# Kernel optimization log

Hardware: AMD Instinct MI355X
Metric: run time of the kernel (lower is better)

Reference implementation:

```python
import jax, jax.numpy as jnp
import numpy as np

B, T, D, NH = 4, 2048, 768, 12
DH = D // NH
NEG = -100000.0  # module uses masked_fill with -100000.0, not -inf


def setup_inputs() -> dict:
    key = jax.random.key(0)
    ks = jax.random.split(key, 9)
    s = 1.0 / np.sqrt(D)
    return {
        "x": jax.random.normal(ks[0], (B, T, D), jnp.float32),
        "wq": jax.random.normal(ks[1], (D, D), jnp.float32) * s,
        "bq": jax.random.normal(ks[2], (D,), jnp.float32) * 0.02,
        "wk": jax.random.normal(ks[3], (D, D), jnp.float32) * s,
        "bk": jax.random.normal(ks[4], (D,), jnp.float32) * 0.02,
        "wv": jax.random.normal(ks[5], (D, D), jnp.float32) * s,
        "bv": jax.random.normal(ks[6], (D,), jnp.float32) * 0.02,
        "wo": jax.random.normal(ks[7], (D, D), jnp.float32) * s,
        "bo": jax.random.normal(ks[8], (D,), jnp.float32) * 0.02,
    }


def reference(x, wq, bq, wk, bk, wv, bv, wo, bo):
    Bx, Tx, E = x.shape
    # torch Linear: y = x @ W.T + b, weight shape [out, in]
    def heads(w, b):
        return (x @ w.T + b).reshape(Bx, Tx, NH, DH).transpose(0, 2, 1, 3)  # [B,nh,T,dh]
    Q, K, V = heads(wq, bq), heads(wk, bk), heads(wv, bv)
    scale = 1.0 / jnp.sqrt(jnp.float32(DH))
    QK = jnp.einsum("bhqd,bhkd->bhqk", Q, K) * scale  # [B,nh,T,T]
    causal = jnp.tril(jnp.ones((Tx, Tx), dtype=bool))
    QK = jnp.where(causal, QK, NEG)
    A = jax.nn.softmax(QK, axis=-1)  # attn_dropout p=0 (eval)
    Z = jnp.einsum("bhqk,bhkd->bhqd", A, V)
    Z = Z.transpose(0, 2, 1, 3).reshape(Bx, Tx, E)
    return Z @ wo.T + bo  # resid_dropout p=0 (eval)
```

## Files before the change

kernel.cpp:

```cpp
#include <hip/hip_runtime.h>


#define B_ 4
#define T_ 2048
#define D_ 768
#define NH_ 12
#define DH_ 64
#define M_ (B_ * T_)

typedef __attribute__((ext_vector_type(8))) short bf16x8;
typedef __attribute__((ext_vector_type(4))) float f32x4;
typedef __attribute__((ext_vector_type(16))) float f32x16;
typedef __attribute__((ext_vector_type(4))) unsigned int u32x4;

__device__ __forceinline__ unsigned short f2bf(float f) {
  unsigned int u = __builtin_bit_cast(unsigned int, f);
  u += 0x7FFFu + ((u >> 16) & 1u);
  return (unsigned short)(u >> 16);
}

__device__ __forceinline__ void async16(const void* g, void* l) {
  __builtin_amdgcn_global_load_lds(
      (const __attribute__((address_space(1))) unsigned int*)g,
      (__attribute__((address_space(3))) unsigned int*)l, 16, 0, 0);
}

#define RAW_BARRIER()                         \
  do {                                        \
    asm volatile("" ::: "memory");            \
    __builtin_amdgcn_s_barrier();             \
    asm volatile("" ::: "memory");            \
  } while (0)

__global__ void cvt_kernel(const float* __restrict__ x, const float* __restrict__ wq,
                           const float* __restrict__ wk, const float* __restrict__ wv,
                           const float* __restrict__ wo,
                           unsigned short* __restrict__ xb, unsigned short* __restrict__ wqb,
                           unsigned short* __restrict__ wkb, unsigned short* __restrict__ wvb,
                           unsigned short* __restrict__ wob) {
  const float* src; unsigned short* dst; int n4;
  switch (blockIdx.y) {
    case 0: src = x;  dst = xb;  n4 = M_ * D_ / 4; break;
    case 1: src = wq; dst = wqb; n4 = D_ * D_ / 4; break;
    case 2: src = wk; dst = wkb; n4 = D_ * D_ / 4; break;
    case 3: src = wv; dst = wvb; n4 = D_ * D_ / 4; break;
    default: src = wo; dst = wob; n4 = D_ * D_ / 4; break;
  }
  int stride = gridDim.x * blockDim.x;
  for (int i = blockIdx.x * blockDim.x + threadIdx.x; i < n4; i += stride) {
    float4 v = ((const float4*)src)[i];
    ushort4 o;
    o.x = f2bf(v.x); o.y = f2bf(v.y); o.z = f2bf(v.z); o.w = f2bf(v.w);
    ((ushort4*)dst)[i] = o;
  }
}

__global__ __launch_bounds__(512, 4) void gemm_kernel(
    const unsigned short* __restrict__ A,
    const unsigned short* __restrict__ W0, const unsigned short* __restrict__ W1,
    const unsigned short* __restrict__ W2,
    const float* __restrict__ bias0, const float* __restrict__ bias1,
    const float* __restrict__ bias2,
    void* out0, void* out1, void* out2,
    float s0, int K, int qkv) {
  __shared__ __align__(16) char lds[49152];

  int bid = blockIdx.x;
  int xcd = bid & 7, g = bid >> 3;
  int mt, nt;
  if (qkv) { mt = xcd + (g / 9) * 8; nt = g % 9; }
  else     { mt = xcd + (g / 3) * 8; nt = g % 3; }
  int y  = qkv ? nt / 3 : 0;
  int nW = qkv ? nt % 3 : nt;
  const unsigned short* W = y == 0 ? W0 : (y == 1 ? W1 : W2);
  const float* bias = y == 0 ? bias0 : (y == 1 ? bias1 : bias2);
  void* outp = y == 0 ? out0 : (y == 1 ? out1 : out2);
  float scl = (qkv && y == 0) ? s0 : 1.0f;
  int mode = qkv ? ((y == 2) ? 2 : 1) : 0;

  int tid = threadIdx.x, lane = tid & 63, wid = tid >> 6;
  int l15 = lane & 15, l4 = lane >> 4;
  int wm = wid >> 2, wn = wid & 3;
  int m0 = mt << 7, n0w = nW << 8;

  int aRow, aCol;
  {
    int row = wid * 16 + (lane >> 2);
    int colE = (lane & 3) * 8;
    aRow = row;
    aCol = colE ^ (((row >> 1) & 3) << 3);
  }
  int bRow[2], bCol[2];
#pragma unroll
  for (int c = 0; c < 2; ++c) {
    int u = c * 8 + wid;
    int row = u * 16 + (lane >> 2);
    int colE = (lane & 3) * 8;
    bRow[c] = row;
    bCol[c] = colE ^ (((row >> 1) & 3) << 3);
  }

  int aoff[4], boff[4];
#pragma unroll
  for (int mf = 0; mf < 4; ++mf) {
    int row = wm * 64 + mf * 16 + l15;
    aoff[mf] = row * 64 + ((l4 * 16) ^ (((row >> 1) & 3) << 4));
  }
#pragma unroll
  for (int nf = 0; nf < 4; ++nf) {
    int row = wn * 64 + nf * 16 + l15;
    boff[nf] = 8192 + row * 64 + ((l4 * 16) ^ (((row >> 1) & 3) << 4));
  }

  const unsigned short* Wb = W + (size_t)n0w * K;

#define ISSUE_TILE(kt, slot)                                                       \
  do {                                                                             \
    async16(A + (size_t)(m0 + aRow) * K + (kt) + aCol, (slot) + wid * 1024);       \
    _Pragma("unroll") for (int c = 0; c < 2; ++c)                                  \
      async16(Wb + (size_t)bRow[c] * K + (kt) + bCol[c],                           \
              (slot) + 8192 + (c * 8 + wid) * 1024);                               \
  } while (0)

  f32x4 acc[4][4] = {};
  char* slot0 = lds;
  char* slot1 = lds + 24576;

  ISSUE_TILE(0, slot0);

  int NT = K >> 5;
#pragma unroll 1
  for (int t = 0; t < NT; ++t) {
    char* cur = (t & 1) ? slot1 : slot0;
    char* nxt = (t & 1) ? slot0 : slot1;
    RAW_BARRIER();
    if (t + 1 < NT) {
      ISSUE_TILE((t + 1) << 5, nxt);
      asm volatile("s_waitcnt vmcnt(3)" ::: "memory");
    } else {
      asm volatile("s_waitcnt vmcnt(0)" ::: "memory");
    }
    RAW_BARRIER();
    bf16x8 af[4], bfr[4];
#pragma unroll
    for (int mf = 0; mf < 4; ++mf) af[mf] = *(const bf16x8*)(cur + aoff[mf]);
#pragma unroll
    for (int nf = 0; nf < 4; ++nf) bfr[nf] = *(const bf16x8*)(cur + boff[nf]);
    __builtin_amdgcn_s_setprio(1);
#pragma unroll
    for (int mf = 0; mf < 4; ++mf)
#pragma unroll
      for (int nf = 0; nf < 4; ++nf)
        acc[mf][nf] = __builtin_amdgcn_mfma_f32_16x16x32_bf16(af[mf], bfr[nf], acc[mf][nf], 0, 0, 0);
    __builtin_amdgcn_s_setprio(0);
  }
#undef ISSUE_TILE

  if (mode == 2) {
#pragma unroll
    for (int nf = 0; nf < 4; ++nf) {
      int colW = n0w + wn * 64 + nf * 16 + l15;
      float bv = bias[colW];
      int h = colW >> 6, d = colW & 63;
#pragma unroll
      for (int mf = 0; mf < 4; ++mf) {
        int rbase = m0 + wm * 64 + mf * 16 + l4 * 4;
        int bb = rbase >> 11, tt = rbase & (T_ - 1);
        ushort4 o;
        o.x = f2bf(acc[mf][nf][0] + bv);
        o.y = f2bf(acc[mf][nf][1] + bv);
        o.z = f2bf(acc[mf][nf][2] + bv);
        o.w = f2bf(acc[mf][nf][3] + bv);
        *(ushort4*)((unsigned short*)outp + ((size_t)(bb * NH_ + h) * DH_ + d) * T_ + tt) = o;
      }
    }
  } else {
#pragma unroll
    for (int nf = 0; nf < 4; ++nf) {
      int colW = n0w + wn * 64 + nf * 16 + l15;
      float bv = bias[colW];
#pragma unroll
      for (int mf = 0; mf < 4; ++mf) {
        int rbase = m0 + wm * 64 + mf * 16 + l4 * 4;
#pragma unroll
        for (int r = 0; r < 4; ++r) {
          float v = (acc[mf][nf][r] + bv) * scl;
          size_t idx = (size_t)(rbase + r) * D_ + colW;
          if (mode == 1) ((unsigned short*)outp)[idx] = f2bf(v);
          else           ((float*)outp)[idx] = v;
        }
      }
    }
  }
}

__global__ __launch_bounds__(256, 2) void attn_kernel(
    const unsigned short* __restrict__ Q, const unsigned short* __restrict__ Kg,
    const unsigned short* __restrict__ VT, unsigned short* __restrict__ Z) {
  __shared__ __align__(16) char lds[49152];

  int tid = threadIdx.x, lane = tid & 63, w = tid >> 6;
  int l31 = lane & 31, hi = lane >> 5;
  int bid = blockIdx.x;
  int xcd = bid & 7, g = bid >> 3;
  int qt = 15 - g / 6;
  int bh = xcd + (g % 6) * 8;
  int b = bh / NH_, h = bh % NH_;
  int q0 = qt * 128;
  int qrow = q0 + w * 32 + l31;

  const unsigned short* Qb = Q + (size_t)(b * T_) * D_ + h * DH_;
  const unsigned short* Kb = Kg + (size_t)(b * T_) * D_ + h * DH_;
  const unsigned short* VTb = VT + (size_t)(b * NH_ + h) * DH_ * T_;

  bf16x8 qf[4];
#pragma unroll
  for (int s = 0; s < 4; ++s)
    qf[s] = *(const bf16x8*)(Qb + (size_t)qrow * D_ + s * 16 + hi * 8);

  int sRow[2], sCol[2];
#pragma unroll
  for (int c = 0; c < 2; ++c) {
    int pos = ((c * 4 + w) * 64 + lane) * 8;
    int row = pos >> 6, colE = pos & 63;
    sRow[c] = row;
    sCol[c] = colE ^ ((row & 7) << 3);
  }

  int koff[2][4];
#pragma unroll
  for (int n = 0; n < 2; ++n)
#pragma unroll
    for (int s = 0; s < 4; ++s) {
      int row = n * 32 + l31;
      koff[n][s] = row * 128 + ((s * 32 + hi * 16) ^ ((row & 7) << 4));
    }

  f32x16 zt[2] = {};
  float l_run = 0.f;
  int ntiles = 2 * qt + 2;

#pragma unroll
  for (int c = 0; c < 2; ++c) {
    async16(Kb + (size_t)sRow[c] * D_ + sCol[c], lds + 0 + (c * 4 + w) * 1024);
    async16(VTb + (size_t)sRow[c] * T_ + sCol[c], lds + 16384 + (c * 4 + w) * 1024);
  }

#define ATTN_TILE(KCUR, VCUR, KNXT, VNXT)                                              \
  do {                                                                                 \
    __syncthreads();          \
    if (t + 1 < ntiles) {                                                              \
      int kv1 = (t + 1) * 64;                                                          \
      _Pragma("unroll") for (int c = 0; c < 2; ++c) {                                  \
        async16(Kb + (size_t)(kv1 + sRow[c]) * D_ + sCol[c],                           \
                lds + KNXT + (c * 4 + w) * 1024);                                      \
        async16(VTb + (size_t)sRow[c] * T_ + kv1 + sCol[c],                            \
                lds + VNXT + (c * 4 + w) * 1024);                                      \
      }                                                                                \
    }                                                                                  \
    f32x16 st[2];                                                                      \
    __builtin_amdgcn_s_setprio(1);                                                     \
    _Pragma("unroll") for (int n = 0; n < 2; ++n) {                                    \
      f32x16 a = {};                                                                   \
      _Pragma("unroll") for (int s = 0; s < 4; ++s) {                                  \
        bf16x8 kf = *(const bf16x8*)(lds + KCUR + koff[n][s]);                         \
        a = __builtin_amdgcn_mfma_f32_32x32x16_bf16(kf, qf[s], a, 0, 0, 0);            \
      }                                                                                \
      st[n] = a;                                                                       \
    }                                                                                  \
    __builtin_amdgcn_s_setprio(0);                                                     \
    if (t >= 2 * qt) {                            \
      int kvb = t * 64;                                                                \
      _Pragma("unroll") for (int n = 0; n < 2; ++n)                                    \
        _Pragma("unroll") for (int m = 0; m < 4; ++m)                                  \
          _Pragma("unroll") for (int c2 = 0; c2 < 4; ++c2) {                           \
            int kv = kvb + n * 32 + m * 8 + hi * 4 + c2;                               \
            if (kv > qrow) st[n][m * 4 + c2] = -1e30f;                                 \
          }                                                                            \
    }                                                                                  \
    bf16x8 pb[4];                                                                      \
    _Pragma("unroll") for (int n = 0; n < 2; ++n) {                                    \
      float u[16];                                                                     \
      _Pragma("unroll") for (int r = 0; r < 16; ++r) {                                 \
        u[r] = __builtin_amdgcn_exp2f(st[n][r]);                                       \
        l_run += u[r];                                                                 \
      }                                                                                \
      _Pragma("unroll") for (int hf = 0; hf < 2; ++hf) {                               \
        unsigned int A0, A1, B0, B1;                                                   \
        asm("v_cvt_pk_bf16_f32 %0, %1, %2" : "=v"(A0) : "v"(u[hf*8+0]), "v"(u[hf*8+1]));\
        asm("v_cvt_pk_bf16_f32 %0, %1, %2" : "=v"(A1) : "v"(u[hf*8+2]), "v"(u[hf*8+3]));\
        asm("v_cvt_pk_bf16_f32 %0, %1, %2" : "=v"(B0) : "v"(u[hf*8+4]), "v"(u[hf*8+5]));\
        asm("v_cvt_pk_bf16_f32 %0, %1, %2" : "=v"(B1) : "v"(u[hf*8+6]), "v"(u[hf*8+7]));\
        asm("v_permlane32_swap_b32 %0, %1" : "+v"(A0), "+v"(B0));                      \
        asm("v_permlane32_swap_b32 %0, %1" : "+v"(A1), "+v"(B1));                      \
        u32x4 pk; pk[0] = A0; pk[1] = A1; pk[2] = B0; pk[3] = B1;                      \
        pb[n * 2 + hf] = __builtin_bit_cast(bf16x8, pk);                               \
      }                                                                                \
    }                                                                                  \
    __builtin_amdgcn_s_setprio(1);                                                     \
    _Pragma("unroll") for (int dt = 0; dt < 2; ++dt) {                                 \
      _Pragma("unroll") for (int s = 0; s < 4; ++s) {                                  \
        bf16x8 vf = *(const bf16x8*)(lds + VCUR + koff[dt][s]);                        \
        zt[dt] = __builtin_amdgcn_mfma_f32_32x32x16_bf16(vf, pb[s], zt[dt], 0, 0, 0);  \
      }                                                                                \
    }                                                                                  \
    __builtin_amdgcn_s_setprio(0);                                                     \
  } while (0)

#pragma unroll 1
  for (int t = 0; t < ntiles; ++t) {
    if ((t & 1) == 0) {
      ATTN_TILE(0, 16384, 8192, 24576);
    } else {
      ATTN_TILE(8192, 24576, 0, 16384);
    }
  }
#undef ATTN_TILE

  l_run += __shfl_xor(l_run, 32);
  float inv = __builtin_amdgcn_rcpf(l_run);
  unsigned short* Zrow = Z + (size_t)(b * T_ + qrow) * D_ + h * DH_;
#pragma unroll
  for (int dt = 0; dt < 2; ++dt)
#pragma unroll
    for (int m = 0; m < 4; ++m) {
      ushort4 o;
      o.x = f2bf(zt[dt][m * 4 + 0] * inv);
      o.y = f2bf(zt[dt][m * 4 + 1] * inv);
      o.z = f2bf(zt[dt][m * 4 + 2] * inv);
      o.w = f2bf(zt[dt][m * 4 + 3] * inv);
      *(ushort4*)(Zrow + dt * 32 + m * 8 + hi * 4) = o;
    }
}

extern "C" void kernel_launch(void* const* d_in, const int* in_sizes, int n_in,
                              void* d_out, int out_size, void* d_ws, size_t ws_size,
                              hipStream_t stream) {
  (void)in_sizes; (void)n_in; (void)out_size; (void)ws_size;
  const float* x  = (const float*)d_in[0];
  const float* wq = (const float*)d_in[1];
  const float* bq = (const float*)d_in[2];
  const float* wk = (const float*)d_in[3];
  const float* bk = (const float*)d_in[4];
  const float* wv = (const float*)d_in[5];
  const float* bv = (const float*)d_in[6];
  const float* wo = (const float*)d_in[7];
  const float* bo = (const float*)d_in[8];

  char* ws = (char*)d_ws;
  const size_t XB = (size_t)M_ * D_ * 2;
  const size_t WB = (size_t)D_ * D_ * 2;
  unsigned short* xb  = (unsigned short*)(ws);
  unsigned short* wqb = (unsigned short*)(ws + XB);
  unsigned short* wkb = (unsigned short*)(ws + XB + WB);
  unsigned short* wvb = (unsigned short*)(ws + XB + 2 * WB);
  unsigned short* wob = (unsigned short*)(ws + XB + 3 * WB);
  unsigned short* Qb  = (unsigned short*)(ws + XB + 4 * WB);
  unsigned short* Kb  = (unsigned short*)(ws + XB + 4 * WB + XB);
  unsigned short* VTb = (unsigned short*)(ws + XB + 4 * WB + 2 * XB);
  unsigned short* Zb  = xb;

  const float SCALE_Q = 0.125f * 1.44269504f;

  cvt_kernel<<<dim3(1024, 5), 256, 0, stream>>>(x, wq, wk, wv, wo, xb, wqb, wkb, wvb, wob);
  gemm_kernel<<<dim3(576), 512, 0, stream>>>(
      xb, wqb, wkb, wvb, bq, bk, bv, Qb, Kb, VTb, SCALE_Q, D_, 1);
  attn_kernel<<<dim3(768), 256, 0, stream>>>(Qb, Kb, VTb, Zb);
  gemm_kernel<<<dim3(192), 512, 0, stream>>>(
      Zb, wob, wob, wob, bo, bo, bo, d_out, d_out, d_out, 1.0f, D_, 0);
}
```

Measured before the change: 120.9 us.

## Use 256x256 tiles with 8-phase pipelined K loop for QKV projection GEMM

Adds a separate QKV GEMM kernel that uses 256x256 output tiles and 64-wide K stages in 128 KB of LDS. The K loop is split into eight phases that interleave async global-to-LDS staging with MFMA work, halving the grid to 288 blocks. The larger tile raises arithmetic intensity per loaded byte. In exchange it lowers occupancy to two blocks per CU and makes the barrier and waitcnt scheduling more intricate. The output-projection GEMM is reduced to a simpler single-purpose kernel.

```diff
diff --git a/kernel.cpp b/kernel.cpp
--- a/kernel.cpp
+++ b/kernel.cpp
@@ -55,7 +55,7 @@
   }
 }
 
-__global__ __launch_bounds__(512, 4) void gemm_kernel(
+__global__ __launch_bounds__(512, 2) void gemm8p_kernel(
     const unsigned short* __restrict__ A,
     const unsigned short* __restrict__ W0, const unsigned short* __restrict__ W1,
     const unsigned short* __restrict__ W2,
@@ -63,7 +63,7 @@
     const float* __restrict__ bias2,
     void* out0, void* out1, void* out2,
     float s0, int K, int qkv) {
-  __shared__ __align__(16) char lds[49152];
+  __shared__ __align__(16) char lds[131072];
 
   int bid = blockIdx.x;
   int xcd = bid & 7, g = bid >> 3;
@@ -81,6 +81,149 @@
   int tid = threadIdx.x, lane = tid & 63, wid = tid >> 6;
   int l15 = lane & 15, l4 = lane >> 4;
   int wm = wid >> 2, wn = wid & 3;
+  int m0 = mt << 8, n0w = nW << 8;
+
+  int sRowH[2], sColE[2];
+#pragma unroll
+  for (int c = 0; c < 2; ++c) {
+    sRowH[c] = (c * 8 + wid) * 8 + (lane >> 3);
+    sColE[c] = ((lane & 7) * 8) ^ ((lane >> 3) << 3);
+  }
+
+  int aoff[8], boff[4];
+#pragma unroll
+  for (int mf = 0; mf < 8; ++mf) {
+    int row = wm * 128 + mf * 16 + l15;
+    aoff[mf] = row * 128 + ((l4 * 16) ^ ((row & 7) << 4));
+  }
+#pragma unroll
+  for (int nf = 0; nf < 4; ++nf) {
+    int row = wn * 64 + nf * 16 + l15;
+    boff[nf] = row * 128 + ((l4 * 16) ^ ((row & 7) << 4));
+  }
+
+  const unsigned short* Ab = A + (size_t)m0 * K;
+  const unsigned short* Wb = W + (size_t)n0w * K;
+
+#define STG(GPTR, LBASE, HALF, KT)                                                   \
+  do {                                                                               \
+    _Pragma("unroll") for (int c = 0; c < 2; ++c)                                    \
+      async16((GPTR) + (size_t)((HALF) * 128 + sRowH[c]) * K + (KT) + sColE[c],      \
+              lds + (LBASE) + (HALF) * 16384 + (c * 8 + wid) * 1024);                \
+  } while (0)
+
+  f32x4 acc[8][4] = {};
+  bf16x8 bfr[4];
+
+#define PH(RA, RB, KS, MH, SYNC, DOSTG, SGP, SLB, SHALF, SKT)                        \
+  do {                                                                               \
+    if (SYNC) {                                                                      \
+      if (DOSTG) {                                                                   \
+        STG(SGP, SLB, SHALF, SKT);                                                   \
+        asm volatile("s_waitcnt vmcnt(2)" ::: "memory");                             \
+      } else {                                                                       \
+        asm volatile("s_waitcnt vmcnt(0)" ::: "memory");                             \
+      }                                                                              \
+      RAW_BARRIER();                                                                 \
+    } else if (DOSTG) {                                                              \
+      STG(SGP, SLB, SHALF, SKT);                                                     \
+    }                                                                                \
+    bf16x8 af[4];                                                                    \
+    _Pragma("unroll") for (int f = 0; f < 4; ++f)                                    \
+      af[f] = *(const bf16x8*)(lds + (RA) + (aoff[(MH) * 4 + f] ^ ((KS) << 6)));     \
+    if ((MH) == 0) {                                                                 \
+      _Pragma("unroll") for (int f = 0; f < 4; ++f)                                  \
+        bfr[f] = *(const bf16x8*)(lds + (RB) + (boff[f] ^ ((KS) << 6)));             \
+    }                                                                                \
+    RAW_BARRIER();                                                                   \
+    __builtin_amdgcn_s_setprio(1);                                                   \
+    _Pragma("unroll") for (int f = 0; f < 4; ++f)                                    \
+      _Pragma("unroll") for (int nf = 0; nf < 4; ++nf)                               \
+        acc[(MH) * 4 + f][nf] = __builtin_amdgcn_mfma_f32_16x16x32_bf16(             \
+            af[f], bfr[nf], acc[(MH) * 4 + f][nf], 0, 0, 0);                         \
+    __builtin_amdgcn_s_setprio(0);                                                   \
+    RAW_BARRIER();                                                                   \
+  } while (0)
+
+  STG(Ab, 0, 0, 0);
+  STG(Ab, 0, 1, 0);
+  STG(Wb, 65536, 0, 0);
+  STG(Wb, 65536, 1, 0);
+  asm volatile("s_waitcnt vmcnt(0)" ::: "memory");
+  RAW_BARRIER();
+
+  int NIT = K >> 7;
+#pragma unroll 1
+  for (int j = 0; j < NIT; ++j) {
+    int kt1 = (2 * j + 1) << 6;
+    int kt2 = (2 * j + 2) << 6;
+    bool st2 = (j + 1 < NIT);
+    PH(0, 65536, 0, 0, true,  true, Ab, 32768, 0, kt1);
+    PH(0, 65536, 0, 1, false, true, Ab, 32768, 1, kt1);
+    PH(0, 65536, 1, 0, false, true, Wb, 98304, 0, kt1);
+    PH(0, 65536, 1, 1, false, true, Wb, 98304, 1, kt1);
+    PH(32768, 98304, 0, 0, true,  st2, Ab, 0, 0, kt2);
+    PH(32768, 98304, 0, 1, false, st2, Ab, 0, 1, kt2);
+    PH(32768, 98304, 1, 0, false, st2, Wb, 65536, 0, kt2);
+    PH(32768, 98304, 1, 1, false, st2, Wb, 65536, 1, kt2);
+  }
+#undef PH
+#undef STG
+
+  if (mode == 2) {
+#pragma unroll
+    for (int nf = 0; nf < 4; ++nf) {
+      int colW = n0w + wn * 64 + nf * 16 + l15;
+      float bv = bias[colW];
+      int h = colW >> 6, d = colW & 63;
+#pragma unroll
+      for (int mf = 0; mf < 8; ++mf) {
+        int rbase = m0 + wm * 128 + mf * 16 + l4 * 4;
+        int bb = rbase >> 11, tt = rbase & (T_ - 1);
+        ushort4 o;
+        o.x = f2bf(acc[mf][nf][0] + bv);
+        o.y = f2bf(acc[mf][nf][1] + bv);
+        o.z = f2bf(acc[mf][nf][2] + bv);
+        o.w = f2bf(acc[mf][nf][3] + bv);
+        *(ushort4*)((unsigned short*)outp + ((size_t)(bb * NH_ + h) * DH_ + d) * T_ + tt) = o;
+      }
+    }
+  } else {
+#pragma unroll
+    for (int nf = 0; nf < 4; ++nf) {
+      int colW = n0w + wn * 64 + nf * 16 + l15;
+      float bv = bias[colW];
+#pragma unroll
+      for (int mf = 0; mf < 8; ++mf) {
+        int rbase = m0 + wm * 128 + mf * 16 + l4 * 4;
+#pragma unroll
+        for (int r = 0; r < 4; ++r) {
+          float v = (acc[mf][nf][r] + bv) * scl;
+          size_t idx = (size_t)(rbase + r) * D_ + colW;
+          if (mode == 1) ((unsigned short*)outp)[idx] = f2bf(v);
+          else           ((float*)outp)[idx] = v;
+        }
+      }
+    }
+  }
+}
+
+__global__ __launch_bounds__(512, 4) void gemm_kernel(
+    const unsigned short* __restrict__ A,
+    const unsigned short* __restrict__ W0,
+    const float* __restrict__ bias0,
+    void* out0, int K) {
+  __shared__ __align__(16) char lds[49152];
+
+  int bid = blockIdx.x;
+  int xcd = bid & 7, g = bid >> 3;
+  int mt = xcd + (g / 3) * 8, nW = g % 3;
+  const unsigned short* W = W0;
+  const float* bias = bias0;
+
+  int tid = threadIdx.x, lane = tid & 63, wid = tid >> 6;
+  int l15 = lane & 15, l4 = lane >> 4;
+  int wm = wid >> 2, wn = wid & 3;
   int m0 = mt << 7, n0w = nW << 8;
 
   int aRow, aCol;
@@ -93,13 +236,10 @@
   int bRow[2], bCol[2];
 #pragma unroll
   for (int c = 0; c < 2; ++c) {
-    int u = c * 8 + wid;
-    int row = u * 16 + (lane >> 2);
-    int colE = (lane & 3) * 8;
+    int row = (c * 8 + wid) * 16 + (lane >> 2);
     bRow[c] = row;
-    bCol[c] = colE ^ (((row >> 1) & 3) << 3);
-  }
-
+    bCol[c] = ((lane & 3) * 8) ^ (((row >> 1) & 3) << 3);
+  }
   int aoff[4], boff[4];
 #pragma unroll
   for (int mf = 0; mf < 4; ++mf) {
@@ -125,7 +265,6 @@
   f32x4 acc[4][4] = {};
   char* slot0 = lds;
   char* slot1 = lds + 24576;
-
   ISSUE_TILE(0, slot0);
 
   int NT = K >> 5;
@@ -156,39 +295,17 @@
   }
 #undef ISSUE_TILE
 
-  if (mode == 2) {
-#pragma unroll
-    for (int nf = 0; nf < 4; ++nf) {
-      int colW = n0w + wn * 64 + nf * 16 + l15;
-      float bv = bias[colW];
-      int h = colW >> 6, d = colW & 63;
-#pragma unroll
-      for (int mf = 0; mf < 4; ++mf) {
-        int rbase = m0 + wm * 64 + mf * 16 + l4 * 4;
-        int bb = rbase >> 11, tt = rbase & (T_ - 1);
-        ushort4 o;
-        o.x = f2bf(acc[mf][nf][0] + bv);
-        o.y = f2bf(acc[mf][nf][1] + bv);
-        o.z = f2bf(acc[mf][nf][2] + bv);
-        o.w = f2bf(acc[mf][nf][3] + bv);
-        *(ushort4*)((unsigned short*)outp + ((size_t)(bb * NH_ + h) * DH_ + d) * T_ + tt) = o;
-      }
-    }
-  } else {
-#pragma unroll
-    for (int nf = 0; nf < 4; ++nf) {
-      int colW = n0w + wn * 64 + nf * 16 + l15;
-      float bv = bias[colW];
-#pragma unroll
-      for (int mf = 0; mf < 4; ++mf) {
-        int rbase = m0 + wm * 64 + mf * 16 + l4 * 4;
-#pragma unroll
-        for (int r = 0; r < 4; ++r) {
-          float v = (acc[mf][nf][r] + bv) * scl;
-          size_t idx = (size_t)(rbase + r) * D_ + colW;
-          if (mode == 1) ((unsigned short*)outp)[idx] = f2bf(v);
-          else           ((float*)outp)[idx] = v;
-        }
+#pragma unroll
+  for (int nf = 0; nf < 4; ++nf) {
+    int colW = n0w + wn * 64 + nf * 16 + l15;
+    float bv = bias[colW];
+#pragma unroll
+    for (int mf = 0; mf < 4; ++mf) {
+      int rbase = m0 + wm * 64 + mf * 16 + l4 * 4;
+#pragma unroll
+      for (int r = 0; r < 4; ++r) {
+        float v = acc[mf][nf][r] + bv;
+        ((float*)out0)[(size_t)(rbase + r) * D_ + colW] = v;
       }
     }
   }
@@ -248,7 +365,7 @@
 
 #define ATTN_TILE(KCUR, VCUR, KNXT, VNXT)                                              \
   do {                                                                                 \
-    __syncthreads();          \
+    __syncthreads();                                                                   \
     if (t + 1 < ntiles) {                                                              \
       int kv1 = (t + 1) * 64;                                                          \
       _Pragma("unroll") for (int c = 0; c < 2; ++c) {                                  \
@@ -269,7 +386,7 @@
       st[n] = a;                                                                       \
     }                                                                                  \
     __builtin_amdgcn_s_setprio(0);                                                     \
-    if (t >= 2 * qt) {                            \
+    if (t >= 2 * qt) {                                                                 \
       int kvb = t * 64;                                                                \
       _Pragma("unroll") for (int n = 0; n < 2; ++n)                                    \
         _Pragma("unroll") for (int m = 0; m < 4; ++m)                                  \
@@ -363,9 +480,8 @@
   const float SCALE_Q = 0.125f * 1.44269504f;
 
   cvt_kernel<<<dim3(1024, 5), 256, 0, stream>>>(x, wq, wk, wv, wo, xb, wqb, wkb, wvb, wob);
-  gemm_kernel<<<dim3(576), 512, 0, stream>>>(
+  gemm8p_kernel<<<dim3(288), 512, 0, stream>>>(
       xb, wqb, wkb, wvb, bq, bk, bv, Qb, Kb, VTb, SCALE_Q, D_, 1);
   attn_kernel<<<dim3(768), 256, 0, stream>>>(Qb, Kb, VTb, Zb);
-  gemm_kernel<<<dim3(192), 512, 0, stream>>>(
-      Zb, wob, wob, wob, bo, bo, bo, d_out, d_out, d_out, 1.0f, D_, 0);
-}
+  gemm_kernel<<<dim3(192), 512, 0, stream>>>(Zb, wob, bo, d_out, D_);
+}
```

New measurement: 135.0 us. 11.7% more time.
